# Performance work log

Hardware: AMD Instinct MI355X
Metric: run time of the kernel (lower is better)

The kernel has to match this reference:

```python
import jax, jax.numpy as jnp
import numpy as np

BSZ, D = 64, 65536
N_NODES, N_FEATS, EMBED_DIM = 1024, 256, 256


def setup_inputs() -> dict:
    key = jax.random.key(0)
    k1, k2, k3, k4, k5, k6 = jax.random.split(key, 6)
    flat_inputs = jax.random.normal(k1, (BSZ, D), dtype=jnp.float32)
    node_ids = jax.random.randint(k2, (BSZ, D), 0, N_NODES, dtype=jnp.int64 if jax.config.jax_enable_x64 else jnp.int32)
    feat_ids = jax.random.randint(k3, (BSZ, D), 0, N_FEATS, dtype=jnp.int64 if jax.config.jax_enable_x64 else jnp.int32)
    # Linear(n_feats -> embed_dim): W is (embed_dim, n_feats) like torch, plus bias.
    lim = 1.0 / np.sqrt(N_FEATS)
    W = jax.random.uniform(k4, (EMBED_DIM, N_FEATS), minval=-lim, maxval=lim, dtype=jnp.float32)
    b = jax.random.uniform(k5, (EMBED_DIM,), minval=-lim, maxval=lim, dtype=jnp.float32)
    global_emb = jax.random.normal(k6, (N_NODES, EMBED_DIM), dtype=jnp.float32)
    return {"flat_inputs": flat_inputs, "node_ids": node_ids, "feat_ids": feat_ids,
            "W": W, "b": b, "global_emb": global_emb}


def _expand(vals, node_ids, feat_ids, n_nodes, n_feats):
    # scatter-fill a dense (bsz, n_nodes, n_feats) tensor (zeros elsewhere)
    bsz, d = vals.shape
    batch_ids = jnp.broadcast_to(jnp.arange(bsz)[:, None], (bsz, d))
    out = jnp.zeros((bsz, n_nodes, n_feats), dtype=vals.dtype)
    return out.at[batch_ids.ravel(), node_ids.ravel(), feat_ids.ravel()].set(vals.ravel())


def reference(flat_inputs, node_ids, feat_ids, W, b, global_emb):
    obs_mat = _expand(flat_inputs, node_ids, feat_ids, N_NODES, N_FEATS)
    mask_mat = _expand(jnp.ones_like(flat_inputs), node_ids, feat_ids, N_NODES, N_FEATS)
    obs_counts = mask_mat.sum(-1, keepdims=True)            # (bsz, n_nodes, 1)
    obs_masked = jnp.nan_to_num((obs_mat * mask_mat) / obs_counts)
    missing_node_mask = obs_counts == 0
    # nodewise Linear + global embedding broadcast over batch
    embedded = jnp.einsum('bnf,ef->bne', obs_masked, W) + b + global_emb[None, :, :]
    return embedded, missing_node_mask
```

## Files before the change

kernel.cpp:

```cpp
#include <hip/hip_runtime.h>
#include <hip/hip_bf16.h>

#define BSZ    64
#define DLEN   65536
#define NNODES 1024
#define NFEATS 256
#define EDIM   256
#define NROWS  (BSZ * NNODES)

#define NRANGE  16
#define NBUCKET (BSZ * NRANGE)
#define LCAP    320
#define GCAP    4600
#define WPAD    268
#define CW      132
#define TW      260

typedef __bf16 bf16x8 __attribute__((ext_vector_type(8)));
typedef float  f32x4  __attribute__((ext_vector_type(4)));

__device__ __forceinline__ unsigned short f2bf(float x) {
  union { float f; unsigned u; } c; c.f = x;
  unsigned r = c.u + 0x7FFFu + ((c.u >> 16) & 1u);
  return (unsigned short)(r >> 16);
}

__global__ __launch_bounds__(512, 8) void bucket_kernel(
    const float* __restrict__ x, const int* __restrict__ nid,
    const int* __restrict__ fid, unsigned* __restrict__ gcnt,
    uint2* __restrict__ gbuf,
    const float* __restrict__ W, unsigned short* __restrict__ Wb) {
  __shared__ uint2 lbuf[NRANGE][LCAP];
  __shared__ unsigned lcnt[NRANGE];
  __shared__ unsigned lbase[NRANGE];

  const int t = threadIdx.x;
  if (t < NRANGE) lcnt[t] = 0;

  if (blockIdx.x < 32) {
    int wi = (blockIdx.x * 512 + t) * 4;
    float4 w = *(const float4*)(W + wi);
    ushort4 o;
    o.x = f2bf(w.x); o.y = f2bf(w.y); o.z = f2bf(w.z); o.w = f2bf(w.w);
    *(ushort4*)(Wb + wi) = o;
  }
  __syncthreads();

  const int b = blockIdx.x >> 4;
  const int base = blockIdx.x * 4096;

#pragma unroll
  for (int k = 0; k < 2; ++k) {
    int i = base + (k * 512 + t) * 4;
    float4 xv = *(const float4*)(x + i);
    int4   nv = *(const int4*)(nid + i);
    int4   fv = *(const int4*)(fid + i);
    int   nd[4] = {nv.x, nv.y, nv.z, nv.w};
    int   ft[4] = {fv.x, fv.y, fv.z, fv.w};
    float vl[4] = {xv.x, xv.y, xv.z, xv.w};
#pragma unroll
    for (int j = 0; j < 4; ++j) {
      int d = (i + j) & 0xFFFF;
      unsigned pack = (((unsigned)(d + 1)) << 15) | ((unsigned)f2bf(vl[j]) >> 1);
      int r = nd[j] >> 6;
      unsigned row = (unsigned)(nd[j] & 63);
      uint2 rec;
      rec.x = pack;
      rec.y = (row << 16) | (row * WPAD + (unsigned)ft[j]);
      unsigned li = atomicAdd(&lcnt[r], 1u);
      if (li < LCAP) {
        lbuf[r][li] = rec;
      } else {
        unsigned gi = atomicAdd(&gcnt[b * NRANGE + r], 1u);
        if (gi < GCAP) gbuf[(size_t)(b * NRANGE + r) * GCAP + gi] = rec;
      }
    }
  }
  __syncthreads();

  if (t < NRANGE) {
    unsigned n = lcnt[t]; if (n > LCAP) n = LCAP;
    lcnt[t] = n;
    lbase[t] = atomicAdd(&gcnt[b * NRANGE + t], n);
  }
  __syncthreads();

  for (int r = 0; r < NRANGE; ++r) {
    unsigned n  = lcnt[r];
    unsigned bs = lbase[r];
    uint2* dst = gbuf + (size_t)(b * NRANGE + r) * GCAP;
    for (unsigned j = t; j < n; j += 512) {
      unsigned gi = bs + j;
      if (gi < GCAP) dst[gi] = lbuf[r][j];
    }
  }
}

__global__ __launch_bounds__(512, 4) void fused_kernel(
    const unsigned* __restrict__ gcnt, const uint2* __restrict__ gbuf,
    const unsigned short* __restrict__ Wb, const float* __restrict__ bias,
    const float* __restrict__ gemb,
    float* __restrict__ out_emb, float* __restrict__ out_mask) {
  __shared__ __align__(16) unsigned win[64 * WPAD];
  __shared__ float scl[64];

  const int t = threadIdx.x;
  const int g = blockIdx.x;
  const int row0 = g * 64;
  const int nb = (g & 15) * 64;

  int cn = (int)gcnt[g]; if (cn > GCAP) cn = GCAP;
  const uint2* bk = gbuf + (size_t)g * GCAP;
  const uint4* bk4 = (const uint4*)bk;
  int np = cn >> 1;
  uint4 r0, r1, r2, r3, r4;
  bool v0 = t < np, v1 = t + 512 < np, v2 = t + 1024 < np,
       v3 = t + 1536 < np, v4 = t + 2048 < np;
  if (v0) r0 = bk4[t];
  if (v1) r1 = bk4[t + 512];
  if (v2) r2 = bk4[t + 1024];
  if (v3) r3 = bk4[t + 1536];
  if (v4) r4 = bk4[t + 2048];

#pragma unroll
  for (int k = 0; k < 8; ++k) {
    int idx = t + k * 512;
    *(uint4*)&win[(idx >> 6) * WPAD + (idx & 63) * 4] = make_uint4(0u, 0u, 0u, 0u);
  }
  __syncthreads();

  if (v0) { atomicMax(&win[r0.y & 0xFFFFu], r0.x); atomicMax(&win[r0.w & 0xFFFFu], r0.z); }
  if (v1) { atomicMax(&win[r1.y & 0xFFFFu], r1.x); atomicMax(&win[r1.w & 0xFFFFu], r1.z); }
  if (v2) { atomicMax(&win[r2.y & 0xFFFFu], r2.x); atomicMax(&win[r2.w & 0xFFFFu], r2.z); }
  if (v3) { atomicMax(&win[r3.y & 0xFFFFu], r3.x); atomicMax(&win[r3.w & 0xFFFFu], r3.z); }
  if (v4) { atomicMax(&win[r4.y & 0xFFFFu], r4.x); atomicMax(&win[r4.w & 0xFFFFu], r4.z); }
  if ((cn & 1) && t == 0) {
    uint2 rec = bk[cn - 1];
    atomicMax(&win[rec.y & 0xFFFFu], rec.x);
  }
  __syncthreads();

  const int lr  = t >> 3;
  const int seg = t & 7;
  uint4 rg[8];
  {
    const uint4* rowp = (const uint4*)&win[lr * WPAD];
    int c = 0;
#pragma unroll
    for (int j = 0; j < 8; ++j) {
      rg[j] = rowp[seg + 8 * j];
      c += (rg[j].x != 0u) + (rg[j].y != 0u) + (rg[j].z != 0u) + (rg[j].w != 0u);
    }
    c += __shfl_down(c, 4, 8);
    c += __shfl_down(c, 2, 8);
    c += __shfl_down(c, 1, 8);
    if (seg == 0) {
      scl[lr] = c ? 1.0f / (float)c : 0.0f;
      out_mask[row0 + lr] = c ? 0.0f : 1.0f;
    }
  }
  __syncthreads();

#pragma unroll
  for (int j = 0; j < 8; ++j) {
    unsigned w0 = ((rg[j].x & 0x7FFFu) << 1) | ((rg[j].y & 0x7FFFu) << 17);
    unsigned w1 = ((rg[j].z & 0x7FFFu) << 1) | ((rg[j].w & 0x7FFFu) << 17);
    *(uint2*)&win[lr * CW + (seg + 8 * j) * 2] = make_uint2(w0, w1);
  }
  __syncthreads();

  const int wv   = t >> 6;
  const int lane = t & 63;
  const int cl   = lane & 15;
  const int q    = lane >> 4;
  const int col0 = wv * 32;

  f32x4 acc[4][2];
#pragma unroll
  for (int mt = 0; mt < 4; ++mt)
#pragma unroll
    for (int nt = 0; nt < 2; ++nt) acc[mt][nt] = (f32x4)(0.0f);

#pragma unroll
  for (int ks = 0; ks < 8; ++ks) {
    bf16x8 bfr[2];
#pragma unroll
    for (int nt = 0; nt < 2; ++nt) {
      const uint4* wp = (const uint4*)(Wb + (size_t)(col0 + nt * 16 + cl) * NFEATS + ks * 32 + q * 8);
      bfr[nt] = __builtin_bit_cast(bf16x8, *wp);
    }
#pragma unroll
    for (int mt = 0; mt < 4; ++mt) {
      bf16x8 afr = __builtin_bit_cast(bf16x8,
          *(const uint4*)&win[(mt * 16 + cl) * CW + ks * 16 + q * 4]);
#pragma unroll
      for (int nt = 0; nt < 2; ++nt)
        acc[mt][nt] = __builtin_amdgcn_mfma_f32_16x16x32_bf16(afr, bfr[nt], acc[mt][nt], 0, 0, 0);
    }
  }
  __syncthreads();

  {
    float* winf = (float*)win;
#pragma unroll
    for (int nt = 0; nt < 2; ++nt) {
      int col = col0 + nt * 16 + cl;
#pragma unroll
      for (int mt = 0; mt < 4; ++mt) {
#pragma unroll
        for (int r2 = 0; r2 < 4; ++r2) {
          int row = mt * 16 + q * 4 + r2;
          winf[row * TW + col] = acc[mt][nt][r2] * scl[row];
        }
      }
    }
  }
  __syncthreads();

  {
    const float* winf = (const float*)win;
#pragma unroll
    for (int k = 0; k < 8; ++k) {
      int f = t + k * 512;
      int row = f >> 6, cg = (f & 63) * 4;
      float4 a  = *(const float4*)&winf[row * TW + cg];
      float4 gv = *(const float4*)&gemb[(size_t)(nb + row) * EDIM + cg];
      float4 bv = *(const float4*)&bias[cg];
      float4 o;
      o.x = a.x + bv.x + gv.x;
      o.y = a.y + bv.y + gv.y;
      o.z = a.z + bv.z + gv.z;
      o.w = a.w + bv.w + gv.w;
      *(float4*)&out_emb[(size_t)(row0 + row) * EDIM + cg] = o;
    }
  }
}

extern "C" void kernel_launch(void* const* d_in, const int* in_sizes, int n_in,
                              void* d_out, int out_size, void* d_ws, size_t ws_size,
                              hipStream_t stream) {
  const float* x    = (const float*)d_in[0];
  const int*   nid  = (const int*)d_in[1];
  const int*   fid  = (const int*)d_in[2];
  const float* W    = (const float*)d_in[3];
  const float* bias = (const float*)d_in[4];
  const float* gemb = (const float*)d_in[5];

  float* out_emb  = (float*)d_out;
  float* out_mask = out_emb + (size_t)NROWS * EDIM;

  unsigned* gcnt = (unsigned*)d_ws;
  uint2* gbuf = (uint2*)((char*)d_ws + 8192);
  unsigned short* Wb = (unsigned short*)((char*)d_ws + 8192 + (size_t)NBUCKET * GCAP * sizeof(uint2));

  hipMemsetAsync(gcnt, 0, NBUCKET * sizeof(unsigned), stream);
  bucket_kernel<<<(BSZ * DLEN) / 4096, 512, 0, stream>>>(x, nid, fid, gcnt, gbuf, W, Wb);
  fused_kernel<<<NBUCKET, 512, 0, stream>>>(gcnt, gbuf, Wb, bias, gemb, out_emb, out_mask);
}
```

Measured before the change: 150.5 us.

## Use 1024-thread blocks in fused kernel and per-wave bucket flush

The fused kernel now runs 1024 threads per block. Each wave computes a 64x16 output strip with half the accumulators, and the scatter, count and epilogue loops are re-split across twice as many threads. In the bucket kernel, the final flush assigns two ranges to each wave instead of looping over all ranges with the whole block. The aim is more parallelism and latency hiding per block and fewer serialized flush iterations. The cost is that each 16-column W fragment is now loaded by more waves, and a larger block occupies a whole CU's worth of threads.

```diff
diff --git a/kernel.cpp b/kernel.cpp
--- a/kernel.cpp
+++ b/kernel.cpp
@@ -85,18 +85,21 @@
   }
   __syncthreads();
 
-  for (int r = 0; r < NRANGE; ++r) {
+  const int wv = t >> 6, lane = t & 63;
+#pragma unroll
+  for (int rr = 0; rr < 2; ++rr) {
+    int r = wv * 2 + rr;
     unsigned n  = lcnt[r];
     unsigned bs = lbase[r];
     uint2* dst = gbuf + (size_t)(b * NRANGE + r) * GCAP;
-    for (unsigned j = t; j < n; j += 512) {
+    for (unsigned j = lane; j < n; j += 64) {
       unsigned gi = bs + j;
       if (gi < GCAP) dst[gi] = lbuf[r][j];
     }
   }
 }
 
-__global__ __launch_bounds__(512, 4) void fused_kernel(
+__global__ __launch_bounds__(1024, 8) void fused_kernel(
     const unsigned* __restrict__ gcnt, const uint2* __restrict__ gbuf,
     const unsigned short* __restrict__ Wb, const float* __restrict__ bias,
     const float* __restrict__ gemb,
@@ -113,18 +116,15 @@
   const uint2* bk = gbuf + (size_t)g * GCAP;
   const uint4* bk4 = (const uint4*)bk;
   int np = cn >> 1;
-  uint4 r0, r1, r2, r3, r4;
-  bool v0 = t < np, v1 = t + 512 < np, v2 = t + 1024 < np,
-       v3 = t + 1536 < np, v4 = t + 2048 < np;
+  uint4 r0, r1, r2;
+  bool v0 = t < np, v1 = t + 1024 < np, v2 = t + 2048 < np;
   if (v0) r0 = bk4[t];
-  if (v1) r1 = bk4[t + 512];
-  if (v2) r2 = bk4[t + 1024];
-  if (v3) r3 = bk4[t + 1536];
-  if (v4) r4 = bk4[t + 2048];
-
-#pragma unroll
-  for (int k = 0; k < 8; ++k) {
-    int idx = t + k * 512;
+  if (v1) r1 = bk4[t + 1024];
+  if (v2) r2 = bk4[t + 2048];
+
+#pragma unroll
+  for (int k = 0; k < 4; ++k) {
+    int idx = t + k * 1024;
     *(uint4*)&win[(idx >> 6) * WPAD + (idx & 63) * 4] = make_uint4(0u, 0u, 0u, 0u);
   }
   __syncthreads();
@@ -132,28 +132,27 @@
   if (v0) { atomicMax(&win[r0.y & 0xFFFFu], r0.x); atomicMax(&win[r0.w & 0xFFFFu], r0.z); }
   if (v1) { atomicMax(&win[r1.y & 0xFFFFu], r1.x); atomicMax(&win[r1.w & 0xFFFFu], r1.z); }
   if (v2) { atomicMax(&win[r2.y & 0xFFFFu], r2.x); atomicMax(&win[r2.w & 0xFFFFu], r2.z); }
-  if (v3) { atomicMax(&win[r3.y & 0xFFFFu], r3.x); atomicMax(&win[r3.w & 0xFFFFu], r3.z); }
-  if (v4) { atomicMax(&win[r4.y & 0xFFFFu], r4.x); atomicMax(&win[r4.w & 0xFFFFu], r4.z); }
   if ((cn & 1) && t == 0) {
     uint2 rec = bk[cn - 1];
     atomicMax(&win[rec.y & 0xFFFFu], rec.x);
   }
   __syncthreads();
 
-  const int lr  = t >> 3;
-  const int seg = t & 7;
-  uint4 rg[8];
+  const int lr  = t >> 4;
+  const int seg = t & 15;
+  uint4 rg[4];
   {
     const uint4* rowp = (const uint4*)&win[lr * WPAD];
     int c = 0;
 #pragma unroll
-    for (int j = 0; j < 8; ++j) {
-      rg[j] = rowp[seg + 8 * j];
+    for (int j = 0; j < 4; ++j) {
+      rg[j] = rowp[seg + 16 * j];
       c += (rg[j].x != 0u) + (rg[j].y != 0u) + (rg[j].z != 0u) + (rg[j].w != 0u);
     }
-    c += __shfl_down(c, 4, 8);
-    c += __shfl_down(c, 2, 8);
-    c += __shfl_down(c, 1, 8);
+    c += __shfl_down(c, 8, 16);
+    c += __shfl_down(c, 4, 16);
+    c += __shfl_down(c, 2, 16);
+    c += __shfl_down(c, 1, 16);
     if (seg == 0) {
       scl[lr] = c ? 1.0f / (float)c : 0.0f;
       out_mask[row0 + lr] = c ? 0.0f : 1.0f;
@@ -162,10 +161,10 @@
   __syncthreads();
 
 #pragma unroll
-  for (int j = 0; j < 8; ++j) {
+  for (int j = 0; j < 4; ++j) {
     unsigned w0 = ((rg[j].x & 0x7FFFu) << 1) | ((rg[j].y & 0x7FFFu) << 17);
     unsigned w1 = ((rg[j].z & 0x7FFFu) << 1) | ((rg[j].w & 0x7FFFu) << 17);
-    *(uint2*)&win[lr * CW + (seg + 8 * j) * 2] = make_uint2(w0, w1);
+    *(uint2*)&win[lr * CW + (seg + 16 * j) * 2] = make_uint2(w0, w1);
   }
   __syncthreads();
 
@@ -173,29 +172,22 @@
   const int lane = t & 63;
   const int cl   = lane & 15;
   const int q    = lane >> 4;
-  const int col0 = wv * 32;
-
-  f32x4 acc[4][2];
-#pragma unroll
-  for (int mt = 0; mt < 4; ++mt)
-#pragma unroll
-    for (int nt = 0; nt < 2; ++nt) acc[mt][nt] = (f32x4)(0.0f);
+  const int col0 = wv * 16;
+  const int col  = col0 + cl;
+
+  f32x4 acc[4];
+#pragma unroll
+  for (int mt = 0; mt < 4; ++mt) acc[mt] = (f32x4)(0.0f);
 
 #pragma unroll
   for (int ks = 0; ks < 8; ++ks) {
-    bf16x8 bfr[2];
-#pragma unroll
-    for (int nt = 0; nt < 2; ++nt) {
-      const uint4* wp = (const uint4*)(Wb + (size_t)(col0 + nt * 16 + cl) * NFEATS + ks * 32 + q * 8);
-      bfr[nt] = __builtin_bit_cast(bf16x8, *wp);
-    }
+    bf16x8 bfr = __builtin_bit_cast(bf16x8,
+        *(const uint4*)(Wb + (size_t)col * NFEATS + ks * 32 + q * 8));
 #pragma unroll
     for (int mt = 0; mt < 4; ++mt) {
       bf16x8 afr = __builtin_bit_cast(bf16x8,
           *(const uint4*)&win[(mt * 16 + cl) * CW + ks * 16 + q * 4]);
-#pragma unroll
-      for (int nt = 0; nt < 2; ++nt)
-        acc[mt][nt] = __builtin_amdgcn_mfma_f32_16x16x32_bf16(afr, bfr[nt], acc[mt][nt], 0, 0, 0);
+      acc[mt] = __builtin_amdgcn_mfma_f32_16x16x32_bf16(afr, bfr, acc[mt], 0, 0, 0);
     }
   }
   __syncthreads();
@@ -203,15 +195,11 @@
   {
     float* winf = (float*)win;
 #pragma unroll
-    for (int nt = 0; nt < 2; ++nt) {
-      int col = col0 + nt * 16 + cl;
-#pragma unroll
-      for (int mt = 0; mt < 4; ++mt) {
-#pragma unroll
-        for (int r2 = 0; r2 < 4; ++r2) {
-          int row = mt * 16 + q * 4 + r2;
-          winf[row * TW + col] = acc[mt][nt][r2] * scl[row];
-        }
+    for (int mt = 0; mt < 4; ++mt) {
+#pragma unroll
+      for (int r2i = 0; r2i < 4; ++r2i) {
+        int row = mt * 16 + q * 4 + r2i;
+        winf[row * TW + col] = acc[mt][r2i] * scl[row];
       }
     }
   }
@@ -220,8 +208,8 @@
   {
     const float* winf = (const float*)win;
 #pragma unroll
-    for (int k = 0; k < 8; ++k) {
-      int f = t + k * 512;
+    for (int k = 0; k < 4; ++k) {
+      int f = t + k * 1024;
       int row = f >> 6, cg = (f & 63) * 4;
       float4 a  = *(const float4*)&winf[row * TW + cg];
       float4 gv = *(const float4*)&gemb[(size_t)(nb + row) * EDIM + cg];
@@ -255,5 +243,5 @@
 
   hipMemsetAsync(gcnt, 0, NBUCKET * sizeof(unsigned), stream);
   bucket_kernel<<<(BSZ * DLEN) / 4096, 512, 0, stream>>>(x, nid, fid, gcnt, gbuf, W, Wb);
-  fused_kernel<<<NBUCKET, 512, 0, stream>>>(gcnt, gbuf, Wb, bias, gemb, out_emb, out_mask);
-}
+  fused_kernel<<<NBUCKET, 1024, 0, stream>>>(gcnt, gbuf, Wb, bias, gemb, out_emb, out_mask);
+}
```

Measured after the change: 145.2 us. 3.5% less time.
